# Kernel optimization log

Hardware: AMD Instinct MI355X
Metric: run time of the kernel (lower is better)

The kernel has to match this reference:

```python
import jax, jax.numpy as jnp
import numpy as np
import math

N, T, D = 4, 2048, 1024

def setup_inputs() -> dict:
    key = jax.random.key(0)
    ks = jax.random.split(key, 14)
    s = 1.0 / math.sqrt(D)
    p = {
        'X':  jax.random.normal(ks[0], (N, T, D), jnp.float32),
        'Wq': jax.random.uniform(ks[1], (D, D), jnp.float32, -s, s),
        'bq': jax.random.uniform(ks[2], (D,), jnp.float32, -s, s),
        'Wk': jax.random.uniform(ks[3], (D, D), jnp.float32, -s, s),
        'bk': jax.random.uniform(ks[4], (D,), jnp.float32, -s, s),
        'Wv': jax.random.uniform(ks[5], (D, D), jnp.float32, -s, s),
        'bv': jax.random.uniform(ks[6], (D,), jnp.float32, -s, s),
        'W1': jax.random.uniform(ks[7], (D, D), jnp.float32, -s, s),
        'b1': jax.random.uniform(ks[8], (D,), jnp.float32, -s, s),
        'W2': jax.random.uniform(ks[9], (D, D), jnp.float32, -s, s),
        'b2': jax.random.uniform(ks[10], (D,), jnp.float32, -s, s),
        'W3': jax.random.uniform(ks[11], (D, D), jnp.float32, -s, s),
        'b3': jax.random.uniform(ks[12], (D,), jnp.float32, -s, s),
        'g1': jnp.ones((D,), jnp.float32),  'be1': jnp.zeros((D,), jnp.float32),
        'g2': jnp.ones((D,), jnp.float32),  'be2': jnp.zeros((D,), jnp.float32),
    }
    return p

def _layer_norm(x, g, b, eps=1e-5):
    mu = jnp.mean(x, axis=-1, keepdims=True)
    var = jnp.mean(jnp.square(x - mu), axis=-1, keepdims=True)
    return (x - mu) * jax.lax.rsqrt(var + eps) * g + b

def reference(X, Wq, bq, Wk, bk, Wv, bv, W1, b1, W2, b2, W3, b3, g1, be1, g2, be2):
    d = X.shape[-1]
    q = X @ Wq + bq                      # (N,T,Dq)
    k = X @ Wk + bk
    v = X @ Wv + bv
    scores = jnp.einsum('ntd,nsd->nts', q, k) / jnp.sqrt(jnp.asarray(d, X.dtype))
    attn = jax.nn.softmax(scores, axis=-1)   # full (N,T,T), as in source
    ctx = jnp.einsum('nts,nsd->ntd', attn, v)
    h = _layer_norm(ctx + X, g1, be1)
    m = jax.nn.relu(h @ W1 + b1)
    m = jax.nn.relu(m @ W2 + b2)
    m = m @ W3 + b3
    return _layer_norm(m + h, g2, be2)
```

## Files before the change

kernel.cpp:

```cpp
#include <hip/hip_runtime.h>
#include <hip/hip_bf16.h>


typedef __attribute__((ext_vector_type(8))) short short8;
typedef __attribute__((ext_vector_type(4))) short short4v;
typedef __attribute__((ext_vector_type(4))) float float4v;

#define DEVI static __device__ __forceinline__

DEVI float bf2f(short s) {
  union { unsigned u; float f; } c;
  c.u = ((unsigned)(unsigned short)s) << 16;
  return c.f;
}
DEVI short f2bf(float f) {
  union { __hip_bfloat16 h; short s; } c;
  c.h = __float2bfloat16(f);
  return c.s;
}
DEVI void gload_lds16(const void* g, void* l) {
  __builtin_amdgcn_global_load_lds(
      (const __attribute__((address_space(1))) void*)g,
      (__attribute__((address_space(3))) void*)l, 16, 0, 0);
}

#define MFMA16 __builtin_amdgcn_mfma_f32_16x16x32_bf16
#define CFENCE asm volatile("" ::: "memory")

__global__ __launch_bounds__(512, 2) void gemm256(
    const short* __restrict__ A, const short* __restrict__ B,
    const float* __restrict__ bias, float alpha, void* __restrict__ Cout,
    int K, int lda, int ldb, int ldc,
    long sA, long sB, long sC, int flags)
{
  __shared__ __attribute__((aligned(16))) short lds[65536];

  const int tid  = threadIdx.x;
  const int lane = tid & 63;
  const int wid  = tid >> 6;
  const int wm = wid >> 2, wn = wid & 3;
  const int lr = lane & 15;
  const int kq = lane >> 4;

  const long m0 = (long)blockIdx.x * 256;
  const long n0 = (long)blockIdx.y * 256;
  const short* Ab = A + (long)blockIdx.z * sA;
  const short* Bb = B + (long)blockIdx.z * sB;

  const int sc8 = (((tid & 7) ^ ((tid >> 3) & 7)) << 3);

  auto stageA = [&](int kt, int half) {
    char* buf = (char*)lds + (kt & 1) * 32768;
    const long k0 = (long)kt * 64 + sc8;
#pragma unroll
    for (int q = 0; q < 2; ++q) {
      const int row = half * 64 + q * 128 + (tid >> 3);
      gload_lds16(Ab + (m0 + row) * (long)lda + k0,
                  buf + half * 8192 + q * 16384 + tid * 16);
    }
  };
  auto stageB = [&](int kt, int half) {
    char* buf = (char*)lds + 65536 + (kt & 1) * 32768;
    const long k0 = (long)kt * 64 + sc8;
#pragma unroll
    for (int q = 0; q < 2; ++q) {
      const int row = half * 32 + (q * 2 + (tid >> 8)) * 64 + ((tid >> 3) & 31);
      gload_lds16(Bb + (n0 + row) * (long)ldb + k0,
                  buf + half * 4096 + q * 16384 + (tid >> 8) * 8192 + (tid & 255) * 16);
    }
  };

  auto rdA = [&](int kt, int fm, int kk) -> short8 {
    const char* buf = (const char*)lds + (kt & 1) * 32768;
    const int row = wm * 128 + fm * 16 + lr;
    const int off = row * 128 + ((((kk << 2) + kq) ^ (lr & 7)) << 4);
    return *(const short8*)(buf + off);
  };
  auto rdB = [&](int kt, int fn, int kk) -> short8 {
    const char* buf = (const char*)lds + 65536 + (kt & 1) * 32768;
    const int row = wn * 64 + fn * 16 + lr;
    const int off = row * 128 + ((((kk << 2) + kq) ^ (lr & 7)) << 4);
    return *(const short8*)(buf + off);
  };

  float4v acc[8][4];
#pragma unroll
  for (int m = 0; m < 8; ++m)
#pragma unroll
    for (int n = 0; n < 4; ++n)
#pragma unroll
      for (int i = 0; i < 4; ++i) acc[m][n][i] = 0.f;

  const int NT = K >> 6;

  stageA(0, 0); stageB(0, 0); stageB(0, 1); stageA(0, 1);
  stageA(1, 0); stageB(1, 0);
  asm volatile("s_waitcnt vmcnt(4)" ::: "memory");
  __builtin_amdgcn_s_barrier();
  CFENCE;

  short8 a0[4][2], a1[4][2], b0[2][2], b1[2][2];

  for (int t = 0; t < NT; ++t) {
#pragma unroll
    for (int m = 0; m < 4; ++m) { a0[m][0] = rdA(t, m, 0); a0[m][1] = rdA(t, m, 1); }
#pragma unroll
    for (int n = 0; n < 2; ++n) { b0[n][0] = rdB(t, n, 0); b0[n][1] = rdB(t, n, 1); }
    if (t + 1 < NT) stageB(t + 1, 1);
    __builtin_amdgcn_s_barrier();
    CFENCE;
    asm volatile("s_waitcnt lgkmcnt(0)" ::: "memory");
    __builtin_amdgcn_sched_barrier(0);
    __builtin_amdgcn_s_setprio(1);
#pragma unroll
    for (int m = 0; m < 4; ++m)
#pragma unroll
      for (int n = 0; n < 2; ++n)
#pragma unroll
        for (int kk = 0; kk < 2; ++kk)
          acc[m][n] = MFMA16(a0[m][kk], b0[n][kk], acc[m][n], 0, 0, 0);
    __builtin_amdgcn_s_setprio(0);

#pragma unroll
    for (int n = 0; n < 2; ++n) { b1[n][0] = rdB(t, n + 2, 0); b1[n][1] = rdB(t, n + 2, 1); }
    if (t + 1 < NT) stageA(t + 1, 1);
    __builtin_amdgcn_s_barrier();
    CFENCE;
    asm volatile("s_waitcnt lgkmcnt(0)" ::: "memory");
    __builtin_amdgcn_sched_barrier(0);
    __builtin_amdgcn_s_setprio(1);
#pragma unroll
    for (int m = 0; m < 4; ++m)
#pragma unroll
      for (int n = 0; n < 2; ++n)
#pragma unroll
        for (int kk = 0; kk < 2; ++kk)
          acc[m][n + 2] = MFMA16(a0[m][kk], b1[n][kk], acc[m][n + 2], 0, 0, 0);
    __builtin_amdgcn_s_setprio(0);

#pragma unroll
    for (int m = 0; m < 4; ++m) { a1[m][0] = rdA(t, m + 4, 0); a1[m][1] = rdA(t, m + 4, 1); }
    if (t + 2 < NT) stageA(t + 2, 0);
    __builtin_amdgcn_s_barrier();
    CFENCE;
    asm volatile("s_waitcnt lgkmcnt(0)" ::: "memory");
    __builtin_amdgcn_sched_barrier(0);
    __builtin_amdgcn_s_setprio(1);
#pragma unroll
    for (int m = 0; m < 4; ++m)
#pragma unroll
      for (int n = 0; n < 2; ++n)
#pragma unroll
        for (int kk = 0; kk < 2; ++kk)
          acc[m + 4][n] = MFMA16(a1[m][kk], b0[n][kk], acc[m + 4][n], 0, 0, 0);
    __builtin_amdgcn_s_setprio(0);

    if (t + 2 < NT) stageB(t + 2, 0);
    if (t + 2 < NT) { asm volatile("s_waitcnt vmcnt(4)" ::: "memory"); }
    else            { asm volatile("s_waitcnt vmcnt(0)" ::: "memory"); }
    __builtin_amdgcn_s_barrier();
    CFENCE;
    __builtin_amdgcn_sched_barrier(0);
    __builtin_amdgcn_s_setprio(1);
#pragma unroll
    for (int m = 0; m < 4; ++m)
#pragma unroll
      for (int n = 0; n < 2; ++n)
#pragma unroll
        for (int kk = 0; kk < 2; ++kk)
          acc[m + 4][n + 2] = MFMA16(a1[m][kk], b1[n][kk], acc[m + 4][n + 2], 0, 0, 0);
    __builtin_amdgcn_s_setprio(0);
  }

  const int dob = flags & 1, dor = flags & 2, f32o = flags & 4;
  float* Cf = (float*)Cout + (long)blockIdx.z * sC;
  short* Cb = (short*)Cout + (long)blockIdx.z * sC;
  const long r0 = m0 + wm * 128 + kq * 4;
  const long c0 = n0 + wn * 64 + lr;
#pragma unroll
  for (int m = 0; m < 8; ++m)
#pragma unroll
    for (int n = 0; n < 4; ++n) {
      const long c = c0 + n * 16;
      float bv = dob ? bias[c] : 0.f;
#pragma unroll
      for (int i = 0; i < 4; ++i) {
        const long r = r0 + m * 16 + i;
        float v = acc[m][n][i] * alpha + bv;
        if (dor) v = fmaxf(v, 0.f);
        if (f32o) Cf[r * ldc + c] = v;
        else      Cb[r * ldc + c] = f2bf(v);
      }
    }
}

__global__ __launch_bounds__(512, 2) void gemm128(
    const short* __restrict__ A, const short* __restrict__ B,
    const float* __restrict__ bias, float alpha, void* __restrict__ Cout,
    int K, int lda, int ldb, int ldc,
    long sA, long sB, long sC, int flags)
{
  __shared__ __attribute__((aligned(16))) short lds[49152];

  const int tid  = threadIdx.x;
  const int lane = tid & 63;
  const int wid  = tid >> 6;
  const int wm = wid >> 1, wn = wid & 1;
  const int lr = lane & 15;
  const int kq = lane >> 4;

  const long m0 = (long)blockIdx.x * 256;
  const long n0 = (long)blockIdx.y * 128;
  const short* Ab = A + (long)blockIdx.z * sA;
  const short* Bb = B + (long)blockIdx.z * sB;

  const int sc8 = (((lane & 7) ^ (lane >> 3)) << 3);

  auto stA = [&](int kt, int half) {
    char* buf = (char*)lds + (kt & 1) * 32768;
    const long k0 = (long)kt * 64 + sc8;
#pragma unroll
    for (int q = 0; q < 2; ++q) {
      const int idx = q * 8 + wid;
      const int rowb = (idx >> 2) * 64 + half * 32 + (idx & 3) * 8;
      gload_lds16(Ab + (m0 + rowb + (lane >> 3)) * (long)lda + k0,
                  buf + rowb * 128 + lane * 16);
    }
  };
  auto stB = [&](int kt, int half) {
    char* buf = (char*)lds + 65536 + (kt & 1) * 16384;
    const long k0 = (long)kt * 64 + sc8;
    const int rowb = (wid >> 2) * 64 + half * 32 + (wid & 3) * 8;
    gload_lds16(Bb + (n0 + rowb + (lane >> 3)) * (long)ldb + k0,
                buf + rowb * 128 + lane * 16);
  };

  auto rdA = [&](int kt, int fm, int kk) -> short8 {
    const char* buf = (const char*)lds + (kt & 1) * 32768;
    const int row = wm * 64 + fm * 16 + lr;
    const int off = row * 128 + ((((kk << 2) + kq) ^ (lr & 7)) << 4);
    return *(const short8*)(buf + off);
  };
  auto rdB = [&](int kt, int fn, int kk) -> short8 {
    const char* buf = (const char*)lds + 65536 + (kt & 1) * 16384;
    const int row = wn * 64 + fn * 16 + lr;
    const int off = row * 128 + ((((kk << 2) + kq) ^ (lr & 7)) << 4);
    return *(const short8*)(buf + off);
  };

  float4v acc[4][4];
#pragma unroll
  for (int m = 0; m < 4; ++m)
#pragma unroll
    for (int n = 0; n < 4; ++n)
#pragma unroll
      for (int i = 0; i < 4; ++i) acc[m][n][i] = 0.f;

  const int NT = K >> 6;

  stA(0, 0); stB(0, 0); stB(0, 1); stA(0, 1);
  asm volatile("s_waitcnt vmcnt(2)" ::: "memory");
  __builtin_amdgcn_s_barrier();
  CFENCE;

  short8 a0[2][2], a1[2][2], b0[2][2], b1[2][2];

  for (int t = 0; t < NT; ++t) {
#pragma unroll
    for (int m = 0; m < 2; ++m) { a0[m][0] = rdA(t, m, 0); a0[m][1] = rdA(t, m, 1); }
#pragma unroll
    for (int n = 0; n < 2; ++n) { b0[n][0] = rdB(t, n, 0); b0[n][1] = rdB(t, n, 1); }
    if (t + 1 < NT) stA(t + 1, 0);
    __builtin_amdgcn_s_barrier();
    CFENCE;
    asm volatile("s_waitcnt lgkmcnt(0)" ::: "memory");
    __builtin_amdgcn_sched_barrier(0);
    __builtin_amdgcn_s_setprio(1);
#pragma unroll
    for (int m = 0; m < 2; ++m)
#pragma unroll
      for (int n = 0; n < 2; ++n)
#pragma unroll
        for (int kk = 0; kk < 2; ++kk)
          acc[m][n] = MFMA16(a0[m][kk], b0[n][kk], acc[m][n], 0, 0, 0);
    __builtin_amdgcn_s_setprio(0);

#pragma unroll
    for (int n = 0; n < 2; ++n) { b1[n][0] = rdB(t, n + 2, 0); b1[n][1] = rdB(t, n + 2, 1); }
    if (t + 1 < NT) { stB(t + 1, 0); stB(t + 1, 1); }
    asm volatile("s_waitcnt vmcnt(4)" ::: "memory");
    __builtin_amdgcn_s_barrier();
    CFENCE;
    asm volatile("s_waitcnt lgkmcnt(0)" ::: "memory");
    __builtin_amdgcn_sched_barrier(0);
    __builtin_amdgcn_s_setprio(1);
#pragma unroll
    for (int m = 0; m < 2; ++m)
#pragma unroll
      for (int n = 0; n < 2; ++n)
#pragma unroll
        for (int kk = 0; kk < 2; ++kk)
          acc[m][n + 2] = MFMA16(a0[m][kk], b1[n][kk], acc[m][n + 2], 0, 0, 0);
    __builtin_amdgcn_s_setprio(0);

#pragma unroll
    for (int m = 0; m < 2; ++m) { a1[m][0] = rdA(t, m + 2, 0); a1[m][1] = rdA(t, m + 2, 1); }
    if (t + 1 < NT) stA(t + 1, 1);
    __builtin_amdgcn_s_barrier();
    CFENCE;
    asm volatile("s_waitcnt lgkmcnt(0)" ::: "memory");
    __builtin_amdgcn_sched_barrier(0);
    __builtin_amdgcn_s_setprio(1);
#pragma unroll
    for (int m = 0; m < 2; ++m)
#pragma unroll
      for (int n = 0; n < 2; ++n)
#pragma unroll
        for (int kk = 0; kk < 2; ++kk)
          acc[m + 2][n] = MFMA16(a1[m][kk], b0[n][kk], acc[m + 2][n], 0, 0, 0);
    __builtin_amdgcn_s_setprio(0);

    if (t + 1 < NT) { asm volatile("s_waitcnt vmcnt(2)" ::: "memory"); }
    else            { asm volatile("s_waitcnt vmcnt(0)" ::: "memory"); }
    __builtin_amdgcn_s_barrier();
    CFENCE;
    __builtin_amdgcn_sched_barrier(0);
    __builtin_amdgcn_s_setprio(1);
#pragma unroll
    for (int m = 0; m < 2; ++m)
#pragma unroll
      for (int n = 0; n < 2; ++n)
#pragma unroll
        for (int kk = 0; kk < 2; ++kk)
          acc[m + 2][n + 2] = MFMA16(a1[m][kk], b1[n][kk], acc[m + 2][n + 2], 0, 0, 0);
    __builtin_amdgcn_s_setprio(0);
  }

  const int dob = flags & 1, dor = flags & 2, f32o = flags & 4;
  float* Cf = (float*)Cout + (long)blockIdx.z * sC;
  short* Cb = (short*)Cout + (long)blockIdx.z * sC;
  const long r0 = m0 + wm * 64 + kq * 4;
  const long c0 = n0 + wn * 64 + lr;
#pragma unroll
  for (int m = 0; m < 4; ++m)
#pragma unroll
    for (int n = 0; n < 4; ++n) {
      const long c = c0 + n * 16;
      float bv = dob ? bias[c] : 0.f;
#pragma unroll
      for (int i = 0; i < 4; ++i) {
        const long r = r0 + m * 16 + i;
        float v = acc[m][n][i] * alpha + bv;
        if (dor) v = fmaxf(v, 0.f);
        if (f32o) Cf[r * ldc + c] = v;
        else      Cb[r * ldc + c] = f2bf(v);
      }
    }
}


__global__ __launch_bounds__(256) void cast_x_k(const float* __restrict__ X,
                                                short* __restrict__ Xb) {
  int i = blockIdx.x * 256 + threadIdx.x;
  float4v v = ((const float4v*)X)[i];
  short4v o;
#pragma unroll
  for (int j = 0; j < 4; ++j) o[j] = f2bf(v[j]);
  ((short4v*)Xb)[i] = o;
}

__global__ __launch_bounds__(256) void twcast_k(const float* __restrict__ W,
                                                short* __restrict__ Wt,
                                                int rows, int cols) {
  __shared__ float tile[32][33];
  int tx = threadIdx.x & 31, ty = threadIdx.x >> 5;
  int c0 = blockIdx.x * 32, r0 = blockIdx.y * 32;
#pragma unroll
  for (int r = ty; r < 32; r += 8)
    tile[r][tx] = W[(long)(r0 + r) * cols + c0 + tx];
  __syncthreads();
#pragma unroll
  for (int r = ty; r < 32; r += 8)
    Wt[(long)(c0 + r) * rows + r0 + tx] = f2bf(tile[tx][r]);
}

__global__ void cbias_k(const float* __restrict__ bq, const float* __restrict__ bk,
                        const float* __restrict__ bv, float* __restrict__ o) {
  int i = blockIdx.x * 256 + threadIdx.x;
  if (i < 1024) o[i] = bq[i];
  else if (i < 2048) o[i] = bk[i - 1024];
  else if (i < 3072) o[i] = bv[i - 2048];
}

__global__ __launch_bounds__(256) void tv_k(const short* __restrict__ qkv,
                                            short* __restrict__ vT) {
  __shared__ short tile[32][33];
  int b = blockIdx.z;
  int tx = threadIdx.x & 31, ty = threadIdx.x >> 5;
  int d0 = blockIdx.x * 32, t0 = blockIdx.y * 32;
#pragma unroll
  for (int r = ty; r < 32; r += 8)
    tile[r][tx] = qkv[((long)(b * 2048 + t0 + r)) * 3072 + 2048 + d0 + tx];
  __syncthreads();
#pragma unroll
  for (int r = ty; r < 32; r += 8)
    vT[(long)b * 2097152 + (long)(d0 + r) * 2048 + t0 + tx] = tile[tx][r];
}

__global__ __launch_bounds__(256) void softmax_k(short* __restrict__ s) {
  __shared__ float red[8];
  long r = blockIdx.x;
  short* p = s + r * 2048;
  int tid = threadIdx.x;
  short8 raw = *(short8*)&p[tid * 8];
  float v[8];
  float mx = -1e30f;
#pragma unroll
  for (int j = 0; j < 8; ++j) { v[j] = bf2f(raw[j]); mx = fmaxf(mx, v[j]); }
#pragma unroll
  for (int o = 32; o; o >>= 1) mx = fmaxf(mx, __shfl_xor(mx, o));
  if ((tid & 63) == 0) red[tid >> 6] = mx;
  __syncthreads();
  mx = fmaxf(fmaxf(red[0], red[1]), fmaxf(red[2], red[3]));
  float sum = 0.f;
#pragma unroll
  for (int j = 0; j < 8; ++j) { v[j] = __expf(v[j] - mx); sum += v[j]; }
#pragma unroll
  for (int o = 32; o; o >>= 1) sum += __shfl_xor(sum, o);
  if ((tid & 63) == 0) red[4 + (tid >> 6)] = sum;
  __syncthreads();
  float inv = 1.f / (red[4] + red[5] + red[6] + red[7]);
  short8 o8;
#pragma unroll
  for (int j = 0; j < 8; ++j) o8[j] = f2bf(v[j] * inv);
  *(short8*)&p[tid * 8] = o8;
}

__global__ __launch_bounds__(256) void addln_k(const float* __restrict__ a,
                                               const float* __restrict__ b,
                                               const float* __restrict__ g,
                                               const float* __restrict__ be,
                                               float* __restrict__ outf,
                                               short* __restrict__ outb) {
  __shared__ float red[8];
  long r = blockIdx.x;
  int tid = threadIdx.x;
  float4v va = ((const float4v*)(a + r * 1024))[tid];
  float4v vb = ((const float4v*)(b + r * 1024))[tid];
  float x[4]; float s = 0.f;
#pragma unroll
  for (int j = 0; j < 4; ++j) { x[j] = va[j] + vb[j]; s += x[j]; }
#pragma unroll
  for (int o = 32; o; o >>= 1) s += __shfl_xor(s, o);
  if ((tid & 63) == 0) red[tid >> 6] = s;
  __syncthreads();
  float mu = (red[0] + red[1] + red[2] + red[3]) * (1.f / 1024.f);
  float ss = 0.f;
#pragma unroll
  for (int j = 0; j < 4; ++j) { float d = x[j] - mu; ss += d * d; }
#pragma unroll
  for (int o = 32; o; o >>= 1) ss += __shfl_xor(ss, o);
  if ((tid & 63) == 0) red[4 + (tid >> 6)] = ss;
  __syncthreads();
  float var = (red[4] + red[5] + red[6] + red[7]) * (1.f / 1024.f);
  float rstd = rsqrtf(var + 1e-5f);
  float4v vg = ((const float4v*)g)[tid];
  float4v vbe = ((const float4v*)be)[tid];
  float4v y;
#pragma unroll
  for (int j = 0; j < 4; ++j) y[j] = (x[j] - mu) * rstd * vg[j] + vbe[j];
  ((float4v*)(outf + r * 1024))[tid] = y;
  if (outb) {
    short4v ob;
#pragma unroll
    for (int j = 0; j < 4; ++j) ob[j] = f2bf(y[j]);
    ((short4v*)(outb + r * 1024))[tid] = ob;
  }
}


extern "C" void kernel_launch(void* const* d_in, const int* in_sizes, int n_in,
                              void* d_out, int out_size, void* d_ws, size_t ws_size,
                              hipStream_t stream) {
  const float* X  = (const float*)d_in[0];
  const float* Wq = (const float*)d_in[1];
  const float* bq = (const float*)d_in[2];
  const float* Wk = (const float*)d_in[3];
  const float* bk = (const float*)d_in[4];
  const float* Wv = (const float*)d_in[5];
  const float* bv = (const float*)d_in[6];
  const float* W1 = (const float*)d_in[7];
  const float* b1 = (const float*)d_in[8];
  const float* W2 = (const float*)d_in[9];
  const float* b2 = (const float*)d_in[10];
  const float* W3 = (const float*)d_in[11];
  const float* b3 = (const float*)d_in[12];
  const float* g1  = (const float*)d_in[13];
  const float* be1 = (const float*)d_in[14];
  const float* g2  = (const float*)d_in[15];
  const float* be2 = (const float*)d_in[16];

  char* ws = (char*)d_ws;
  short* Xb     = (short*)(ws + 0);
  short* Wqkvt  = (short*)(ws + 16777216);
  short* W1t    = (short*)(ws + 23068672);
  short* W2t    = (short*)(ws + 25165824);
  short* W3t    = (short*)(ws + 27262976);
  float* bqkv   = (float*)(ws + 29360128);
  short* qkv    = (short*)(ws + 29372416);
  short* vT     = (short*)(ws + 79704064);
  short* scores = (short*)(ws + 96481280);
  float* ctx    = (float*)(ws + 29372416);
  float* h      = (float*)(ws + 96481280);
  short* hb     = (short*)(ws + 0);
  short* m1     = (short*)(ws + 29372416);
  short* m2     = (short*)(ws + 46149632);
  float* m3     = (float*)(ws + 62926848);
  float* out    = (float*)d_out;

  cast_x_k<<<8192, 256, 0, stream>>>(X, Xb);
  twcast_k<<<dim3(32, 32), 256, 0, stream>>>(Wq, Wqkvt + 0,       1024, 1024);
  twcast_k<<<dim3(32, 32), 256, 0, stream>>>(Wk, Wqkvt + 1048576, 1024, 1024);
  twcast_k<<<dim3(32, 32), 256, 0, stream>>>(Wv, Wqkvt + 2097152, 1024, 1024);
  twcast_k<<<dim3(32, 32), 256, 0, stream>>>(W1, W1t, 1024, 1024);
  twcast_k<<<dim3(32, 32), 256, 0, stream>>>(W2, W2t, 1024, 1024);
  twcast_k<<<dim3(32, 32), 256, 0, stream>>>(W3, W3t, 1024, 1024);
  cbias_k<<<12, 256, 0, stream>>>(bq, bk, bv, bqkv);

  gemm256<<<dim3(32, 12, 1), 512, 0, stream>>>(
      Xb, Wqkvt, bqkv, 1.0f, qkv, 1024, 1024, 1024, 3072, 0, 0, 0, 1);

  tv_k<<<dim3(32, 64, 4), 256, 0, stream>>>(qkv, vT);

  gemm256<<<dim3(8, 8, 4), 512, 0, stream>>>(
      qkv, qkv + 1024, nullptr, 0.03125f, scores, 1024, 3072, 3072, 2048,
      (long)2048 * 3072, (long)2048 * 3072, (long)2048 * 2048, 0);

  softmax_k<<<8192, 256, 0, stream>>>(scores);

  gemm128<<<dim3(8, 8, 4), 512, 0, stream>>>(
      scores, vT, nullptr, 1.0f, ctx, 2048, 2048, 2048, 1024,
      (long)2048 * 2048, (long)1024 * 2048, (long)2048 * 1024, 4);

  addln_k<<<8192, 256, 0, stream>>>(ctx, X, g1, be1, h, hb);

  gemm128<<<dim3(32, 8, 1), 512, 0, stream>>>(
      hb, W1t, b1, 1.0f, m1, 1024, 1024, 1024, 1024, 0, 0, 0, 3);
  gemm128<<<dim3(32, 8, 1), 512, 0, stream>>>(
      m1, W2t, b2, 1.0f, m2, 1024, 1024, 1024, 1024, 0, 0, 0, 3);
  gemm128<<<dim3(32, 8, 1), 512, 0, stream>>>(
      m2, W3t, b3, 1.0f, m3, 1024, 1024, 1024, 1024, 0, 0, 0, 5);

  addln_k<<<8192, 256, 0, stream>>>(m3, h, g2, be2, out, nullptr);
}
```

Before: 317.2 us.

## Restructure GEMM main loops to two barriers per step with LDS prefetch, merge weight casts

```diff
diff --git a/kernel.cpp b/kernel.cpp
--- a/kernel.cpp
+++ b/kernel.cpp
@@ -26,6 +26,7 @@
 
 #define MFMA16 __builtin_amdgcn_mfma_f32_16x16x32_bf16
 #define CFENCE asm volatile("" ::: "memory")
+#define SCHEDB __builtin_amdgcn_sched_barrier(0)
 
 __global__ __launch_bounds__(512, 2) void gemm256(
     const short* __restrict__ A, const short* __restrict__ B,
@@ -100,76 +101,63 @@
   CFENCE;
 
   short8 a0[4][2], a1[4][2], b0[2][2], b1[2][2];
+#pragma unroll
+  for (int m = 0; m < 4; ++m) { a0[m][0] = rdA(0, m, 0); a0[m][1] = rdA(0, m, 1); }
+#pragma unroll
+  for (int n = 0; n < 2; ++n) {
+    b0[n][0] = rdB(0, n, 0);     b0[n][1] = rdB(0, n, 1);
+    b1[n][0] = rdB(0, n + 2, 0); b1[n][1] = rdB(0, n + 2, 1);
+  }
 
   for (int t = 0; t < NT; ++t) {
-#pragma unroll
-    for (int m = 0; m < 4; ++m) { a0[m][0] = rdA(t, m, 0); a0[m][1] = rdA(t, m, 1); }
-#pragma unroll
-    for (int n = 0; n < 2; ++n) { b0[n][0] = rdB(t, n, 0); b0[n][1] = rdB(t, n, 1); }
-    if (t + 1 < NT) stageB(t + 1, 1);
+    if (t + 1 < NT) { stageB(t + 1, 1); stageA(t + 1, 1); }
     __builtin_amdgcn_s_barrier();
     CFENCE;
     asm volatile("s_waitcnt lgkmcnt(0)" ::: "memory");
-    __builtin_amdgcn_sched_barrier(0);
+    SCHEDB;
     __builtin_amdgcn_s_setprio(1);
 #pragma unroll
     for (int m = 0; m < 4; ++m)
 #pragma unroll
       for (int n = 0; n < 2; ++n)
 #pragma unroll
-        for (int kk = 0; kk < 2; ++kk)
-          acc[m][n] = MFMA16(a0[m][kk], b0[n][kk], acc[m][n], 0, 0, 0);
+        for (int kk = 0; kk < 2; ++kk) {
+          acc[m][n]     = MFMA16(a0[m][kk], b0[n][kk], acc[m][n], 0, 0, 0);
+          acc[m][n + 2] = MFMA16(a0[m][kk], b1[n][kk], acc[m][n + 2], 0, 0, 0);
+        }
     __builtin_amdgcn_s_setprio(0);
-
-#pragma unroll
-    for (int n = 0; n < 2; ++n) { b1[n][0] = rdB(t, n + 2, 0); b1[n][1] = rdB(t, n + 2, 1); }
-    if (t + 1 < NT) stageA(t + 1, 1);
-    __builtin_amdgcn_s_barrier();
-    CFENCE;
-    asm volatile("s_waitcnt lgkmcnt(0)" ::: "memory");
-    __builtin_amdgcn_sched_barrier(0);
-    __builtin_amdgcn_s_setprio(1);
-#pragma unroll
-    for (int m = 0; m < 4; ++m)
-#pragma unroll
-      for (int n = 0; n < 2; ++n)
-#pragma unroll
-        for (int kk = 0; kk < 2; ++kk)
-          acc[m][n + 2] = MFMA16(a0[m][kk], b1[n][kk], acc[m][n + 2], 0, 0, 0);
-    __builtin_amdgcn_s_setprio(0);
-
+    SCHEDB;
 #pragma unroll
     for (int m = 0; m < 4; ++m) { a1[m][0] = rdA(t, m + 4, 0); a1[m][1] = rdA(t, m + 4, 1); }
-    if (t + 2 < NT) stageA(t + 2, 0);
-    __builtin_amdgcn_s_barrier();
-    CFENCE;
-    asm volatile("s_waitcnt lgkmcnt(0)" ::: "memory");
-    __builtin_amdgcn_sched_barrier(0);
-    __builtin_amdgcn_s_setprio(1);
-#pragma unroll
-    for (int m = 0; m < 4; ++m)
-#pragma unroll
-      for (int n = 0; n < 2; ++n)
-#pragma unroll
-        for (int kk = 0; kk < 2; ++kk)
-          acc[m + 4][n] = MFMA16(a1[m][kk], b0[n][kk], acc[m + 4][n], 0, 0, 0);
-    __builtin_amdgcn_s_setprio(0);
-
-    if (t + 2 < NT) stageB(t + 2, 0);
+
+    if (t + 2 < NT) { stageA(t + 2, 0); stageB(t + 2, 0); }
     if (t + 2 < NT) { asm volatile("s_waitcnt vmcnt(4)" ::: "memory"); }
     else            { asm volatile("s_waitcnt vmcnt(0)" ::: "memory"); }
     __builtin_amdgcn_s_barrier();
     CFENCE;
-    __builtin_amdgcn_sched_barrier(0);
+    asm volatile("s_waitcnt lgkmcnt(0)" ::: "memory");
+    SCHEDB;
     __builtin_amdgcn_s_setprio(1);
 #pragma unroll
     for (int m = 0; m < 4; ++m)
 #pragma unroll
       for (int n = 0; n < 2; ++n)
 #pragma unroll
-        for (int kk = 0; kk < 2; ++kk)
+        for (int kk = 0; kk < 2; ++kk) {
+          acc[m + 4][n]     = MFMA16(a1[m][kk], b0[n][kk], acc[m + 4][n], 0, 0, 0);
           acc[m + 4][n + 2] = MFMA16(a1[m][kk], b1[n][kk], acc[m + 4][n + 2], 0, 0, 0);
+        }
     __builtin_amdgcn_s_setprio(0);
+    SCHEDB;
+    if (t + 1 < NT) {
+#pragma unroll
+      for (int m = 0; m < 4; ++m) { a0[m][0] = rdA(t + 1, m, 0); a0[m][1] = rdA(t + 1, m, 1); }
+#pragma unroll
+      for (int n = 0; n < 2; ++n) {
+        b0[n][0] = rdB(t + 1, n, 0);     b0[n][1] = rdB(t + 1, n, 1);
+        b1[n][0] = rdB(t + 1, n + 2, 0); b1[n][1] = rdB(t + 1, n + 2, 1);
+      }
+    }
   }
 
   const int dob = flags & 1, dor = flags & 2, f32o = flags & 4;
@@ -264,76 +252,65 @@
   CFENCE;
 
   short8 a0[2][2], a1[2][2], b0[2][2], b1[2][2];
+#pragma unroll
+  for (int m = 0; m < 2; ++m) { a0[m][0] = rdA(0, m, 0); a0[m][1] = rdA(0, m, 1); }
+#pragma unroll
+  for (int n = 0; n < 2; ++n) {
+    b0[n][0] = rdB(0, n, 0);     b0[n][1] = rdB(0, n, 1);
+    b1[n][0] = rdB(0, n + 2, 0); b1[n][1] = rdB(0, n + 2, 1);
+  }
 
   for (int t = 0; t < NT; ++t) {
-#pragma unroll
-    for (int m = 0; m < 2; ++m) { a0[m][0] = rdA(t, m, 0); a0[m][1] = rdA(t, m, 1); }
-#pragma unroll
-    for (int n = 0; n < 2; ++n) { b0[n][0] = rdB(t, n, 0); b0[n][1] = rdB(t, n, 1); }
-    if (t + 1 < NT) stA(t + 1, 0);
+    if (t + 1 < NT) { stA(t + 1, 0); stB(t + 1, 0); stB(t + 1, 1); }
+    if (t + 1 < NT) { asm volatile("s_waitcnt vmcnt(4)" ::: "memory"); }
+    else            { asm volatile("s_waitcnt vmcnt(0)" ::: "memory"); }
     __builtin_amdgcn_s_barrier();
     CFENCE;
     asm volatile("s_waitcnt lgkmcnt(0)" ::: "memory");
-    __builtin_amdgcn_sched_barrier(0);
+    SCHEDB;
     __builtin_amdgcn_s_setprio(1);
 #pragma unroll
     for (int m = 0; m < 2; ++m)
 #pragma unroll
       for (int n = 0; n < 2; ++n)
 #pragma unroll
-        for (int kk = 0; kk < 2; ++kk)
-          acc[m][n] = MFMA16(a0[m][kk], b0[n][kk], acc[m][n], 0, 0, 0);
+        for (int kk = 0; kk < 2; ++kk) {
+          acc[m][n]     = MFMA16(a0[m][kk], b0[n][kk], acc[m][n], 0, 0, 0);
+          acc[m][n + 2] = MFMA16(a0[m][kk], b1[n][kk], acc[m][n + 2], 0, 0, 0);
+        }
     __builtin_amdgcn_s_setprio(0);
-
-#pragma unroll
-    for (int n = 0; n < 2; ++n) { b1[n][0] = rdB(t, n + 2, 0); b1[n][1] = rdB(t, n + 2, 1); }
-    if (t + 1 < NT) { stB(t + 1, 0); stB(t + 1, 1); }
-    asm volatile("s_waitcnt vmcnt(4)" ::: "memory");
-    __builtin_amdgcn_s_barrier();
-    CFENCE;
-    asm volatile("s_waitcnt lgkmcnt(0)" ::: "memory");
-    __builtin_amdgcn_sched_barrier(0);
-    __builtin_amdgcn_s_setprio(1);
-#pragma unroll
-    for (int m = 0; m < 2; ++m)
-#pragma unroll
-      for (int n = 0; n < 2; ++n)
-#pragma unroll
-        for (int kk = 0; kk < 2; ++kk)
-          acc[m][n + 2] = MFMA16(a0[m][kk], b1[n][kk], acc[m][n + 2], 0, 0, 0);
-    __builtin_amdgcn_s_setprio(0);
-
+    SCHEDB;
 #pragma unroll
     for (int m = 0; m < 2; ++m) { a1[m][0] = rdA(t, m + 2, 0); a1[m][1] = rdA(t, m + 2, 1); }
-    if (t + 1 < NT) stA(t + 1, 1);
-    __builtin_amdgcn_s_barrier();
-    CFENCE;
-    asm volatile("s_waitcnt lgkmcnt(0)" ::: "memory");
-    __builtin_amdgcn_sched_barrier(0);
-    __builtin_amdgcn_s_setprio(1);
-#pragma unroll
-    for (int m = 0; m < 2; ++m)
-#pragma unroll
-      for (int n = 0; n < 2; ++n)
-#pragma unroll
-        for (int kk = 0; kk < 2; ++kk)
-          acc[m + 2][n] = MFMA16(a1[m][kk], b0[n][kk], acc[m + 2][n], 0, 0, 0);
-    __builtin_amdgcn_s_setprio(0);
-
+
+    if (t + 1 < NT) { stA(t + 1, 1); }
     if (t + 1 < NT) { asm volatile("s_waitcnt vmcnt(2)" ::: "memory"); }
     else            { asm volatile("s_waitcnt vmcnt(0)" ::: "memory"); }
     __builtin_amdgcn_s_barrier();
     CFENCE;
-    __builtin_amdgcn_sched_barrier(0);
+    asm volatile("s_waitcnt lgkmcnt(0)" ::: "memory");
+    SCHEDB;
     __builtin_amdgcn_s_setprio(1);
 #pragma unroll
     for (int m = 0; m < 2; ++m)
 #pragma unroll
       for (int n = 0; n < 2; ++n)
 #pragma unroll
-        for (int kk = 0; kk < 2; ++kk)
+        for (int kk = 0; kk < 2; ++kk) {
+          acc[m + 2][n]     = MFMA16(a1[m][kk], b0[n][kk], acc[m + 2][n], 0, 0, 0);
           acc[m + 2][n + 2] = MFMA16(a1[m][kk], b1[n][kk], acc[m + 2][n + 2], 0, 0, 0);
+        }
     __builtin_amdgcn_s_setprio(0);
+    SCHEDB;
+    if (t + 1 < NT) {
+#pragma unroll
+      for (int m = 0; m < 2; ++m) { a0[m][0] = rdA(t + 1, m, 0); a0[m][1] = rdA(t + 1, m, 1); }
+#pragma unroll
+      for (int n = 0; n < 2; ++n) {
+        b0[n][0] = rdB(t + 1, n, 0);     b0[n][1] = rdB(t + 1, n, 1);
+        b1[n][0] = rdB(t + 1, n + 2, 0); b1[n][1] = rdB(t + 1, n + 2, 1);
+      }
+    }
   }
 
   const int dob = flags & 1, dor = flags & 2, f32o = flags & 4;
@@ -369,27 +346,35 @@
   ((short4v*)Xb)[i] = o;
 }
 
-__global__ __launch_bounds__(256) void twcast_k(const float* __restrict__ W,
-                                                short* __restrict__ Wt,
-                                                int rows, int cols) {
+__global__ __launch_bounds__(256) void wcast_k(
+    const float* __restrict__ Wq, const float* __restrict__ Wk,
+    const float* __restrict__ Wv, const float* __restrict__ W1,
+    const float* __restrict__ W2, const float* __restrict__ W3,
+    const float* __restrict__ bq, const float* __restrict__ bk,
+    const float* __restrict__ bv,
+    short* __restrict__ Wqkvt, short* __restrict__ W1t,
+    short* __restrict__ W2t, short* __restrict__ W3t,
+    float* __restrict__ bqkv) {
+  const int z = blockIdx.z;
+  if (z == 6) {
+    if (blockIdx.y != 0 || blockIdx.x >= 12) return;
+    int i = blockIdx.x * 256 + threadIdx.x;
+    bqkv[i] = i < 1024 ? bq[i] : (i < 2048 ? bk[i - 1024] : bv[i - 2048]);
+    return;
+  }
+  const float* W = z == 0 ? Wq : z == 1 ? Wk : z == 2 ? Wv : z == 3 ? W1 : z == 4 ? W2 : W3;
+  short* Wt = z == 0 ? Wqkvt : z == 1 ? Wqkvt + 1048576 : z == 2 ? Wqkvt + 2097152
+            : z == 3 ? W1t : z == 4 ? W2t : W3t;
   __shared__ float tile[32][33];
   int tx = threadIdx.x & 31, ty = threadIdx.x >> 5;
   int c0 = blockIdx.x * 32, r0 = blockIdx.y * 32;
 #pragma unroll
   for (int r = ty; r < 32; r += 8)
-    tile[r][tx] = W[(long)(r0 + r) * cols + c0 + tx];
+    tile[r][tx] = W[(long)(r0 + r) * 1024 + c0 + tx];
   __syncthreads();
 #pragma unroll
   for (int r = ty; r < 32; r += 8)
-    Wt[(long)(c0 + r) * rows + r0 + tx] = f2bf(tile[tx][r]);
-}
-
-__global__ void cbias_k(const float* __restrict__ bq, const float* __restrict__ bk,
-                        const float* __restrict__ bv, float* __restrict__ o) {
-  int i = blockIdx.x * 256 + threadIdx.x;
-  if (i < 1024) o[i] = bq[i];
-  else if (i < 2048) o[i] = bk[i - 1024];
-  else if (i < 3072) o[i] = bv[i - 2048];
+    Wt[(long)(c0 + r) * 1024 + r0 + tx] = f2bf(tile[tx][r]);
 }
 
 __global__ __launch_bounds__(256) void tv_k(const short* __restrict__ qkv,
@@ -519,13 +504,9 @@
   float* out    = (float*)d_out;
 
   cast_x_k<<<8192, 256, 0, stream>>>(X, Xb);
-  twcast_k<<<dim3(32, 32), 256, 0, stream>>>(Wq, Wqkvt + 0,       1024, 1024);
-  twcast_k<<<dim3(32, 32), 256, 0, stream>>>(Wk, Wqkvt + 1048576, 1024, 1024);
-  twcast_k<<<dim3(32, 32), 256, 0, stream>>>(Wv, Wqkvt + 2097152, 1024, 1024);
-  twcast_k<<<dim3(32, 32), 256, 0, stream>>>(W1, W1t, 1024, 1024);
-  twcast_k<<<dim3(32, 32), 256, 0, stream>>>(W2, W2t, 1024, 1024);
-  twcast_k<<<dim3(32, 32), 256, 0, stream>>>(W3, W3t, 1024, 1024);
-  cbias_k<<<12, 256, 0, stream>>>(bq, bk, bv, bqkv);
+  wcast_k<<<dim3(32, 32, 7), 256, 0, stream>>>(Wq, Wk, Wv, W1, W2, W3,
+                                               bq, bk, bv,
+                                               Wqkvt, W1t, W2t, W3t, bqkv);
 
   gemm256<<<dim3(32, 12, 1), 512, 0, stream>>>(
       Xb, Wqkvt, bqkv, 1.0f, qkv, 1024, 1024, 1024, 3072, 0, 0, 0, 1);
```

Result: no change. 311.4 us (-1.8%).
